# Kernel optimization log

Measured on AMD Instinct MI355X. Metric: run time of the kernel, lower is better.

## Reference

```python
import jax, jax.numpy as jnp
import numpy as np

B, NC, NF, D = 4, 256, 768, 768
TOK_RATIO = 0.5
LN_EPS = 1e-5


def _linear(x, w, b):
    # w: [D_in, D_out]
    return x @ w + b


def _leaky(x):
    return jax.nn.leaky_relu(x, negative_slope=0.01)


def setup_inputs() -> dict:
    key = jax.random.key(0)
    ks = jax.random.split(key, 12)
    s = 1.0 / np.sqrt(D)
    inp = {
        "cls_tokens": jax.random.normal(ks[0], (B, NC, D), dtype=jnp.float32),
        "feats": jax.random.normal(ks[1], (B, NF, D), dtype=jnp.float32),
        "W_head_w": jax.random.uniform(ks[2], (D, D), minval=-s, maxval=s),
        "W_head_b": jax.random.uniform(ks[3], (D,), minval=-s, maxval=s),
        "W_tail_w": jax.random.uniform(ks[4], (D, D), minval=-s, maxval=s),
        "W_tail_b": jax.random.uniform(ks[5], (D,), minval=-s, maxval=s),
        "lin1_w": jax.random.uniform(ks[6], (D, D), minval=-s, maxval=s),
        "lin1_b": jax.random.uniform(ks[7], (D,), minval=-s, maxval=s),
        "lin2_w": jax.random.uniform(ks[8], (D, D), minval=-s, maxval=s),
        "lin2_b": jax.random.uniform(ks[9], (D,), minval=-s, maxval=s),
        "ln_w": jnp.ones((D,), dtype=jnp.float32),
        "ln_b": jnp.zeros((D,), dtype=jnp.float32),
    }
    return inp


def reference(cls_tokens, feats, W_head_w, W_head_b, W_tail_w, W_tail_b,
              lin1_w, lin1_b, lin2_w, lin2_b, ln_w, ln_b):
    topk = int(TOK_RATIO * NC)
    scale = D ** (-0.5)

    # feats is detached in the original (clone().detach())
    x = jnp.concatenate([cls_tokens, jax.lax.stop_gradient(feats)], axis=1)  # [B, Nt, D]

    e_h = _linear(cls_tokens, W_head_w, W_head_b)  # [B, Nc, D]
    e_t = _linear(x, W_tail_w, W_tail_b)           # [B, Nt, D]

    attn_logit = jnp.einsum('bnd,bmd->bnm', e_h * scale, e_t)  # [B, Nc, Nt]
    topk_weight, topk_index = jax.lax.top_k(attn_logit, topk)  # [B, Nc, k]

    # Gather neighbor embeddings: Nb_h[b, n, j] = e_t[b, topk_index[b, n, j]]
    Nb_h = jax.vmap(lambda et, idx: et[idx])(e_t, topk_index)  # [B, Nc, k, D]

    topk_prob = jax.nn.softmax(topk_weight, axis=2)            # [B, Nc, k]
    p = topk_prob[..., None]
    eh_r = p * Nb_h + (1.0 - p) * e_h[:, :, None, :]           # [B, Nc, k, D]

    gate = jnp.tanh(e_h[:, :, None, :] + eh_r)
    ka_weight = jnp.einsum('bnkd,bnkd->bnk', Nb_h, gate)
    ka_prob = jax.nn.softmax(ka_weight, axis=2)
    e_Nh = jnp.einsum('bnk,bnkd->bnd', ka_prob, Nb_h)          # [B, Nc, D]

    # bi-interaction aggregation
    sum_emb = _leaky(_linear((e_h + e_Nh) * 0.1 + cls_tokens, lin1_w, lin1_b))
    bi_emb = _leaky(_linear(e_h * e_Nh * 0.1 + cls_tokens, lin2_w, lin2_b))
    embedding = sum_emb + bi_emb

    # LayerNorm (dropout is a no-op: p=0 and output overwritten in original)
    mu = jnp.mean(embedding, axis=-1, keepdims=True)
    var = jnp.var(embedding, axis=-1, keepdims=True)
    h = (embedding - mu) * jax.lax.rsqrt(var + LN_EPS) * ln_w + ln_b
    return h
```

## Files before the change

### kernel.cpp

```cpp
#include <hip/hip_runtime.h>
#include <hip/hip_bf16.h>
#include <math.h>

#define DDIM 768
#define NCLS 256
#define NFEAT 768
#define NTOK 1024
#define NBATCH 4
#define KSEL 128

typedef float f32x4 __attribute__((ext_vector_type(4)));
typedef short s16x8 __attribute__((ext_vector_type(8)));

__device__ __forceinline__ float wsum(float v) {
#pragma unroll
  for (int o = 32; o; o >>= 1) v += __shfl_down(v, o, 64);
  return v;
}
__device__ __forceinline__ float wmaxr(float v) {
#pragma unroll
  for (int o = 32; o; o >>= 1) v = fmaxf(v, __shfl_down(v, o, 64));
  return v;
}
__device__ __forceinline__ short f2bf(float f) {
  union { __hip_bfloat16 h; short s; } u;
  u.h = __float2bfloat16(f);
  return u.s;
}
__device__ __forceinline__ float bf2f(short s) {
  union { unsigned u; float f; } c;
  c.u = ((unsigned)(unsigned short)s) << 16;
  return c.f;
}
__device__ __forceinline__ void cvt8(float4 x, float4 y, s16x8& h, s16x8& l) {
  float v[8] = {x.x, x.y, x.z, x.w, y.x, y.y, y.z, y.w};
#pragma unroll
  for (int i = 0; i < 8; ++i) {
    short hh = f2bf(v[i]);
    h[i] = hh;
    l[i] = f2bf(v[i] - bf2f(hh));
  }
}
__device__ __forceinline__ int swz(int row, int chunk) {
  return (row << 5) + (((chunk ^ (row >> 1)) & 3) << 3);
}

__global__ __launch_bounds__(256) void prep_all(
    const float* __restrict__ cls, const float* __restrict__ feats,
    const float* __restrict__ w0, const float* __restrict__ w1,
    const float* __restrict__ w2, const float* __restrict__ w3,
    short* __restrict__ h0, short* __restrict__ h1, short* __restrict__ h2,
    short* __restrict__ h3, short* __restrict__ l0, short* __restrict__ l1,
    short* __restrict__ Xh, short* __restrict__ Xl) {
  __shared__ float tile[32][33];
  const int bid = blockIdx.x;
  const int t = threadIdx.x;
  if (bid < 2304) {
    const int z = bid / 576, rem = bid % 576;
    const int by = rem / 24, bx = rem % 24;
    const float* s = z == 0 ? w0 : z == 1 ? w1 : z == 2 ? w2 : w3;
    short* dh = z == 0 ? h0 : z == 1 ? h1 : z == 2 ? h2 : h3;
    short* dl = z == 0 ? l0 : z == 1 ? l1 : nullptr;
    const int tx = t & 31, ty0 = t >> 5;
    const int r0 = by * 32, c0 = bx * 32;
#pragma unroll
    for (int i = 0; i < 4; ++i) {
      int ty = ty0 + i * 8;
      tile[ty][tx] = s[(size_t)(r0 + ty) * DDIM + c0 + tx];
    }
    __syncthreads();
#pragma unroll
    for (int i = 0; i < 4; ++i) {
      int ty = ty0 + i * 8;
      float v = tile[tx][ty];
      short hh = f2bf(v);
      dh[(size_t)(c0 + ty) * DDIM + r0 + tx] = hh;
      if (dl) dl[(size_t)(c0 + ty) * DDIM + r0 + tx] = f2bf(v - bf2f(hh));
    }
  } else {
    const size_t base = ((size_t)(bid - 2304) * 256 + t) * 8;
    const int row = (int)(base / DDIM);
    const int col = (int)(base % DDIM);
    const int b = row >> 10, rr = row & 1023;
    const float* src =
        (rr < NCLS) ? cls + ((size_t)b * NCLS + rr) * DDIM + col
                    : feats + ((size_t)b * NFEAT + (rr - NCLS)) * DDIM + col;
    float4 a0 = *(const float4*)(src);
    float4 a1 = *(const float4*)(src + 4);
    s16x8 h, l;
    cvt8(a0, a1, h, l);
    *(s16x8*)(Xh + base) = h;
    *(s16x8*)(Xl + base) = l;
  }
}

__global__ __launch_bounds__(256) void gemm_front(
    const short* __restrict__ Xh, const short* __restrict__ Xl,
    const short* __restrict__ WhT_h, const short* __restrict__ WhT_l,
    const float* __restrict__ Whb, const short* __restrict__ WtT_h,
    const short* __restrict__ WtT_l, const float* __restrict__ Wtb,
    short* __restrict__ eh_hi, short* __restrict__ eh_lo,
    short* __restrict__ et_hi, short* __restrict__ et_lo) {
  __shared__ short Ah[128 * 32], Al[128 * 32];
  __shared__ short Bh[64 * 32], Bl[64 * 32];
  const int bid = blockIdx.x;
  const int xcd = bid & 7, idx = bid >> 3;
  const int ytile = xcd * 5 + idx / 12;
  const int xtile = idx % 12;
  const int t = threadIdx.x;
  const int row0 = ytile * 128, col0 = xtile * 64;
  const bool head = row0 < 1024;

  const int ar = t >> 1, ac = (t & 1) * 2;
  const int aw0 = swz(ar, ac), aw1 = swz(ar, ac + 1);
  size_t xrow;
  {
    int gr = row0 + ar;
    xrow = head ? (size_t)(((gr >> 8) << 10) + (gr & 255)) : (size_t)(gr - 1024);
  }
  const short* aph = Xh + xrow * DDIM + ac * 8;
  const short* apl = Xl + xrow * DDIM + ac * 8;
  const int br = t >> 2, bc = t & 3;
  const int bw0 = swz(br, bc);
  const short* bph = (head ? WhT_h : WtT_h) + (size_t)(col0 + br) * DDIM + bc * 8;
  const short* bpl = (head ? WhT_l : WtT_l) + (size_t)(col0 + br) * DDIM + bc * 8;
  const float* biasu = head ? Whb : Wtb;

  const int lane = t & 63, wave = t >> 6;
  const int wr = wave >> 1, wc = wave & 1;
  const int fr = lane & 15, fq = lane >> 4;

  f32x4 acc[4][2] = {};
  s16x8 rah0 = *(const s16x8*)(aph);
  s16x8 rah1 = *(const s16x8*)(aph + 8);
  s16x8 ral0 = *(const s16x8*)(apl);
  s16x8 ral1 = *(const s16x8*)(apl + 8);
  s16x8 rbh = *(const s16x8*)(bph);
  s16x8 rbl = *(const s16x8*)(bpl);

  for (int kt = 0; kt < 24; ++kt) {
    __syncthreads();
    *(s16x8*)&Ah[aw0] = rah0;
    *(s16x8*)&Ah[aw1] = rah1;
    *(s16x8*)&Al[aw0] = ral0;
    *(s16x8*)&Al[aw1] = ral1;
    *(s16x8*)&Bh[bw0] = rbh;
    *(s16x8*)&Bl[bw0] = rbl;
    __syncthreads();
    const int kn = (kt < 23 ? kt + 1 : 23) * 32;
    rah0 = *(const s16x8*)(aph + kn);
    rah1 = *(const s16x8*)(aph + kn + 8);
    ral0 = *(const s16x8*)(apl + kn);
    ral1 = *(const s16x8*)(apl + kn + 8);
    rbh = *(const s16x8*)(bph + kn);
    rbl = *(const s16x8*)(bpl + kn);

    s16x8 afh[4], afl[4];
#pragma unroll
    for (int m = 0; m < 4; ++m) {
      int ao = swz(wr * 64 + m * 16 + fr, fq);
      afh[m] = *(const s16x8*)&Ah[ao];
      afl[m] = *(const s16x8*)&Al[ao];
    }
#pragma unroll
    for (int n = 0; n < 2; ++n) {
      int bo = swz(wc * 32 + n * 16 + fr, fq);
      s16x8 bfh = *(const s16x8*)&Bh[bo];
      s16x8 bfl = *(const s16x8*)&Bl[bo];
#pragma unroll
      for (int m = 0; m < 4; ++m) {
        acc[m][n] =
            __builtin_amdgcn_mfma_f32_16x16x32_bf16(afh[m], bfh, acc[m][n], 0, 0, 0);
        acc[m][n] =
            __builtin_amdgcn_mfma_f32_16x16x32_bf16(afh[m], bfl, acc[m][n], 0, 0, 0);
        acc[m][n] =
            __builtin_amdgcn_mfma_f32_16x16x32_bf16(afl[m], bfh, acc[m][n], 0, 0, 0);
      }
    }
  }

  short* Ch = head ? eh_hi : et_hi;
  short* Cl = head ? eh_lo : et_lo;
  const int rbase = head ? row0 : row0 - 1024;
#pragma unroll
  for (int m = 0; m < 4; ++m) {
#pragma unroll
    for (int n = 0; n < 2; ++n) {
#pragma unroll
      for (int r = 0; r < 4; ++r) {
        int rg = rbase + wr * 64 + m * 16 + fq * 4 + r;
        int cg = col0 + wc * 32 + n * 16 + fr;
        float v = acc[m][n][r] + biasu[cg];
        size_t o = (size_t)rg * DDIM + cg;
        short hh = f2bf(v);
        Ch[o] = hh;
        Cl[o] = f2bf(v - bf2f(hh));
      }
    }
  }
}

__global__ __launch_bounds__(256) void gemm_logits(
    const short* __restrict__ eh_hi, const short* __restrict__ eh_lo,
    const short* __restrict__ et_hi, const short* __restrict__ et_lo,
    float* __restrict__ logits, float scale) {
  __shared__ short Ah[32 * 32], Al[32 * 32];
  __shared__ short Bh[64 * 32], Bl[64 * 32];
  const int bid = blockIdx.x;
  const int xcd = bid & 7, idx = bid >> 3;
  const int batch = xcd >> 1;
  const int sub = ((xcd & 1) << 6) | idx;
  const int xtile = sub & 15, ytile = sub >> 4;
  const int row0 = ytile * 32, col0 = xtile * 64;
  const int t = threadIdx.x;

  const int ahalf = t >> 7, ac2 = t & 127;
  const int asr = ac2 >> 2, acc_ = ac2 & 3;
  const short* aptr = (ahalf ? eh_lo : eh_hi) +
                      ((size_t)batch * NCLS + row0 + asr) * DDIM + acc_ * 8;
  const int aso = swz(asr, acc_);
  const int bsr = t >> 2, bcc = t & 3;
  const short* bph = et_hi + ((size_t)batch * NTOK + col0 + bsr) * DDIM + bcc * 8;
  const short* bpl = et_lo + ((size_t)batch * NTOK + col0 + bsr) * DDIM + bcc * 8;
  const int bso = swz(bsr, bcc);

  const int lane = t & 63, wave = t >> 6;
  const int wr = wave >> 1, wc = wave & 1;
  const int fr = lane & 15, fq = lane >> 4;

  f32x4 acc[2] = {};
  s16x8 rA = *(const s16x8*)(aptr);
  s16x8 rbh = *(const s16x8*)(bph);
  s16x8 rbl = *(const s16x8*)(bpl);

  for (int kt = 0; kt < 24; ++kt) {
    __syncthreads();
    *(s16x8*)&(ahalf ? Al : Ah)[aso] = rA;
    *(s16x8*)&Bh[bso] = rbh;
    *(s16x8*)&Bl[bso] = rbl;
    __syncthreads();
    const int kn = (kt < 23 ? kt + 1 : 23) * 32;
    rA = *(const s16x8*)(aptr + kn);
    rbh = *(const s16x8*)(bph + kn);
    rbl = *(const s16x8*)(bpl + kn);
    int ao = swz(wr * 16 + fr, fq);
    s16x8 afh = *(const s16x8*)&Ah[ao];
    s16x8 afl = *(const s16x8*)&Al[ao];
#pragma unroll
    for (int n = 0; n < 2; ++n) {
      int bo = swz(wc * 32 + n * 16 + fr, fq);
      s16x8 bfh = *(const s16x8*)&Bh[bo];
      s16x8 bfl = *(const s16x8*)&Bl[bo];
      acc[n] = __builtin_amdgcn_mfma_f32_16x16x32_bf16(afh, bfh, acc[n], 0, 0, 0);
      acc[n] = __builtin_amdgcn_mfma_f32_16x16x32_bf16(afh, bfl, acc[n], 0, 0, 0);
      acc[n] = __builtin_amdgcn_mfma_f32_16x16x32_bf16(afl, bfh, acc[n], 0, 0, 0);
    }
  }

  float* Cb = logits + (size_t)batch * NCLS * NTOK;
#pragma unroll
  for (int n = 0; n < 2; ++n)
#pragma unroll
    for (int r = 0; r < 4; ++r) {
      int rg = row0 + wr * 16 + fq * 4 + r;
      int cg = col0 + wc * 32 + n * 16 + fr;
      Cb[(size_t)rg * NTOK + cg] = scale * acc[n][r];
    }
}

__global__ __launch_bounds__(256) void gemm_lin(
    const short* __restrict__ inbf, const short* __restrict__ L1T,
    const short* __restrict__ L2T, const float* __restrict__ b1,
    const float* __restrict__ b2, float* __restrict__ emb) {
  __shared__ short A1[32 * 32], A2[32 * 32];
  __shared__ short B1[64 * 32], B2[64 * 32];
  const int bid = blockIdx.x;
  const int xcd = bid & 7, idx = bid >> 3;
  const int ytile = xcd * 4 + idx / 12, xtile = idx % 12;
  const int t = threadIdx.x;
  const int row0 = ytile * 32, col0 = xtile * 64;

  const int ahalf = t >> 7, at = t & 127;
  const int asr = at >> 2, asc = at & 3;
  const short* aptr = inbf + (ahalf ? (size_t)1024 * DDIM : 0) +
                      (size_t)(row0 + asr) * DDIM + asc * 8;
  const int aso = swz(asr, asc);
  const int bsr = t >> 2, bsc = t & 3;
  const short* b1p = L1T + (size_t)(col0 + bsr) * DDIM + bsc * 8;
  const short* b2p = L2T + (size_t)(col0 + bsr) * DDIM + bsc * 8;
  const int bso = swz(bsr, bsc);

  const int lane = t & 63, wave = t >> 6;
  const int wr = wave >> 1, wc = wave & 1;
  const int fr = lane & 15, fq = lane >> 4;

  f32x4 acc1[2] = {}, acc2[2] = {};
  s16x8 rA = *(const s16x8*)(aptr);
  s16x8 rB1 = *(const s16x8*)(b1p);
  s16x8 rB2 = *(const s16x8*)(b2p);
  for (int kt = 0; kt < 24; ++kt) {
    __syncthreads();
    *(s16x8*)&(ahalf ? A2 : A1)[aso] = rA;
    *(s16x8*)&B1[bso] = rB1;
    *(s16x8*)&B2[bso] = rB2;
    __syncthreads();
    const int kn = (kt < 23 ? kt + 1 : 23) * 32;
    rA = *(const s16x8*)(aptr + kn);
    rB1 = *(const s16x8*)(b1p + kn);
    rB2 = *(const s16x8*)(b2p + kn);
    int ao = swz(wr * 16 + fr, fq);
    s16x8 a1f = *(const s16x8*)&A1[ao];
    s16x8 a2f = *(const s16x8*)&A2[ao];
#pragma unroll
    for (int n = 0; n < 2; ++n) {
      int bo = swz(wc * 32 + n * 16 + fr, fq);
      s16x8 b1f = *(const s16x8*)&B1[bo];
      s16x8 b2f = *(const s16x8*)&B2[bo];
      acc1[n] = __builtin_amdgcn_mfma_f32_16x16x32_bf16(a1f, b1f, acc1[n], 0, 0, 0);
      acc2[n] = __builtin_amdgcn_mfma_f32_16x16x32_bf16(a2f, b2f, acc2[n], 0, 0, 0);
    }
  }
#pragma unroll
  for (int n = 0; n < 2; ++n)
#pragma unroll
    for (int r = 0; r < 4; ++r) {
      int rg = row0 + wr * 16 + fq * 4 + r;
      int cg = col0 + wc * 32 + n * 16 + fr;
      float v1 = acc1[n][r] + b1[cg];
      v1 = v1 > 0.f ? v1 : 0.01f * v1;
      float v2 = acc2[n][r] + b2[cg];
      v2 = v2 > 0.f ? v2 : 0.01f * v2;
      emb[(size_t)rg * DDIM + cg] = v1 + v2;
    }
}

__global__ __launch_bounds__(256) void topk_select(
    const float* __restrict__ logits, float* __restrict__ tw,
    int* __restrict__ ti) {
  const int row = blockIdx.x;
  const int t = threadIdx.x;
  const int lane = t & 63, wave = t >> 6;
  __shared__ int hist[256];
  __shared__ int sh_bin, sh_rem;
  __shared__ int cnt;
  __shared__ int wsumT[4];

  float4 v4 = *(const float4*)(logits + (size_t)row * NTOK + 4 * t);
  float val[4] = {v4.x, v4.y, v4.z, v4.w};
  unsigned key[4];
#pragma unroll
  for (int i = 0; i < 4; ++i) {
    unsigned u = __float_as_uint(val[i]);
    key[i] = (u & 0x80000000u) ? ~u : (u | 0x80000000u);
  }

  unsigned pref = 0, mask = 0;
  int rem = KSEL;
#pragma unroll
  for (int shift = 24; shift >= 0; shift -= 8) {
    hist[t] = 0;
    __syncthreads();
#pragma unroll
    for (int i = 0; i < 4; ++i)
      if ((key[i] & mask) == pref)
        atomicAdd(&hist[(key[i] >> shift) & 255], 1);
    __syncthreads();
    if (wave == 0) {
      int h0 = hist[4 * lane], h1 = hist[4 * lane + 1];
      int h2 = hist[4 * lane + 2], h3 = hist[4 * lane + 3];
      int s = h0 + h1 + h2 + h3;
#pragma unroll
      for (int o = 1; o < 64; o <<= 1) {
        int v = __shfl_down(s, o, 64);
        if (lane + o < 64) s += v;
      }
      int abv = __shfl_down(s, 1, 64);
      if (lane == 63) abv = 0;
      int c3 = abv + h3, c2 = c3 + h2, c1 = c2 + h1, c0 = c1 + h0;
      int bin = -1, nab = 0;
      if (c3 >= rem && abv < rem) { bin = 4 * lane + 3; nab = abv; }
      else if (c2 >= rem && c3 < rem) { bin = 4 * lane + 2; nab = c3; }
      else if (c1 >= rem && c2 < rem) { bin = 4 * lane + 1; nab = c2; }
      else if (c0 >= rem && c1 < rem) { bin = 4 * lane + 0; nab = c1; }
      if (bin >= 0) { sh_bin = bin; sh_rem = rem - nab; }
    }
    __syncthreads();
    pref |= ((unsigned)sh_bin) << shift;
    mask |= 0xFFu << shift;
    rem = sh_rem;
  }

  const unsigned T = pref;
  const int above = KSEL - rem;

  if (t == 0) cnt = 0;
  int tc = 0;
#pragma unroll
  for (int i = 0; i < 4; ++i) tc += (key[i] == T);
  int inc = tc;
#pragma unroll
  for (int o = 1; o < 64; o <<= 1) {
    int v = __shfl_up(inc, o, 64);
    if (lane >= o) inc += v;
  }
  if (lane == 63) wsumT[wave] = inc;
  __syncthreads();
  int wbase = 0;
#pragma unroll
  for (int w = 0; w < 4; ++w)
    if (w < wave) wbase += wsumT[w];
  int excl = wbase + inc - tc;

  float* twr = tw + (size_t)row * KSEL;
  int* tir = ti + (size_t)row * KSEL;
#pragma unroll
  for (int i = 0; i < 4; ++i) {
    if (key[i] > T) {
      int slot = atomicAdd(&cnt, 1);
      twr[slot] = val[i];
      tir[slot] = 4 * t + i;
    } else if (key[i] == T) {
      int r = excl++;
      if (r < rem) {
        twr[above + r] = val[i];
        tir[above + r] = 4 * t + i;
      }
    }
  }
}

__global__ __launch_bounds__(256) void agg1(const short* __restrict__ eh_hi,
                                            const short* __restrict__ et_hi,
                                            const float* __restrict__ tw,
                                            const int* __restrict__ ti,
                                            float* __restrict__ kaw_raw) {
  const int bid = blockIdx.x;
  const int xcd = bid & 7, slot = bid >> 3;
  const int batch = xcd >> 1;
  const int u = ((xcd & 1) << 8) | slot;
  const int row = batch * 256 + (u >> 1);
  const int half = u & 1;
  const int t = threadIdx.x, lane = t & 63, wave = t >> 6;
  __shared__ float p[KSEL];
  __shared__ int idxs[KSEL];
  __shared__ float red[2];

  if (t < KSEL) {
    p[t] = tw[(size_t)row * KSEL + t];
    idxs[t] = ti[(size_t)row * KSEL + t];
  }
  __syncthreads();
  if (wave == 0) {
    float m = wmaxr(fmaxf(p[lane], p[lane + 64]));
    if (!lane) red[0] = m;
  }
  __syncthreads();
  if (t < KSEL) p[t] = __expf(p[t] - red[0]);
  __syncthreads();
  if (wave == 0) {
    float s = wsum(p[lane] + p[lane + 64]);
    if (!lane) red[1] = s;
  }
  __syncthreads();
  if (t < KSEL) p[t] *= (1.f / red[1]);
  __syncthreads();

  float ehr[12];
  {
    const short* ehrow = eh_hi + (size_t)row * DDIM;
    s16x8 e8 = *(const s16x8*)(ehrow + 8 * lane);
    short4 e4 = *(const short4*)(ehrow + 512 + 4 * lane);
#pragma unroll
    for (int i = 0; i < 8; ++i) ehr[i] = bf2f(e8[i]);
    ehr[8] = bf2f(e4.x);
    ehr[9] = bf2f(e4.y);
    ehr[10] = bf2f(e4.z);
    ehr[11] = bf2f(e4.w);
  }
  const short* etb = et_hi + (size_t)batch * NTOK * DDIM;

  for (int i = 0; i < 16; ++i) {
    int j = half * 64 + wave * 16 + i;
    float pj = p[j];
    float a = 4.f - 2.f * pj, b2 = 2.f * pj;
    const short* nb = etb + (size_t)idxs[j] * DDIM;
    s16x8 n8 = *(const s16x8*)(nb + 8 * lane);
    short4 n4 = *(const short4*)(nb + 512 + 4 * lane);
    float nq[12];
#pragma unroll
    for (int q = 0; q < 8; ++q) nq[q] = bf2f(n8[q]);
    nq[8] = bf2f(n4.x);
    nq[9] = bf2f(n4.y);
    nq[10] = bf2f(n4.z);
    nq[11] = bf2f(n4.w);
    float partial = 0.f;
#pragma unroll
    for (int q = 0; q < 12; ++q) {
      float y2 = fmaf(a, ehr[q], b2 * nq[q]);
      float ex = __expf(y2);
      float g = fmaf(-2.f, __builtin_amdgcn_rcpf(1.f + ex), 1.f);
      partial = fmaf(nq[q], g, partial);
    }
    partial = wsum(partial);
    if (!lane) kaw_raw[(size_t)row * KSEL + j] = partial;
  }
}

__global__ __launch_bounds__(192) void agg2(
    const short* __restrict__ eh_hi, const short* __restrict__ et_hi,
    const float* __restrict__ cls, const float* __restrict__ kaw_raw,
    const int* __restrict__ ti, short* __restrict__ inbf) {
  const int bid = blockIdx.x;
  const int xcd = bid & 7, slot = bid >> 3;
  const int batch = xcd >> 1;
  const int row = batch * 256 + (xcd & 1) * 128 + slot;
  const int t = threadIdx.x, lane = t & 63, wave = t >> 6;
  __shared__ float kp[KSEL];
  __shared__ int idxs[KSEL];
  __shared__ float red[2];

  if (t < KSEL) {
    kp[t] = kaw_raw[(size_t)row * KSEL + t];
    idxs[t] = ti[(size_t)row * KSEL + t];
  }
  __syncthreads();
  if (wave == 0) {
    float m = wmaxr(fmaxf(kp[lane], kp[lane + 64]));
    if (!lane) red[0] = m;
  }
  __syncthreads();
  if (t < KSEL) kp[t] = __expf(kp[t] - red[0]);
  __syncthreads();
  if (wave == 0) {
    float s = wsum(kp[lane] + kp[lane + 64]);
    if (!lane) red[1] = s;
  }
  __syncthreads();
  if (t < KSEL) kp[t] *= (1.f / red[1]);
  __syncthreads();

  const size_t o = (size_t)row * DDIM + 4 * t;
  short4 ehs = *(const short4*)(eh_hi + o);
  float4 eh4 = {bf2f(ehs.x), bf2f(ehs.y), bf2f(ehs.z), bf2f(ehs.w)};
  float4 cl4 = *(const float4*)(cls + o);
  const short* etb = et_hi + (size_t)batch * NTOK * DDIM;

  float ax = 0.f, ay = 0.f, az = 0.f, aw = 0.f;
#pragma unroll 8
  for (int j = 0; j < KSEL; ++j) {
    float pr = kp[j];
    short4 nb = *(const short4*)(etb + (size_t)idxs[j] * DDIM + 4 * t);
    ax = fmaf(pr, bf2f(nb.x), ax);
    ay = fmaf(pr, bf2f(nb.y), ay);
    az = fmaf(pr, bf2f(nb.z), az);
    aw = fmaf(pr, bf2f(nb.w), aw);
  }

  short4 sv, bv;
  sv.x = f2bf((eh4.x + ax) * 0.1f + cl4.x);
  sv.y = f2bf((eh4.y + ay) * 0.1f + cl4.y);
  sv.z = f2bf((eh4.z + az) * 0.1f + cl4.z);
  sv.w = f2bf((eh4.w + aw) * 0.1f + cl4.w);
  bv.x = f2bf((eh4.x * ax) * 0.1f + cl4.x);
  bv.y = f2bf((eh4.y * ay) * 0.1f + cl4.y);
  bv.z = f2bf((eh4.z * az) * 0.1f + cl4.z);
  bv.w = f2bf((eh4.w * aw) * 0.1f + cl4.w);
  *(short4*)&inbf[o] = sv;
  *(short4*)&inbf[(size_t)(NBATCH * NCLS) * DDIM + o] = bv;
}

__global__ __launch_bounds__(256) void ln_kernel(const float* __restrict__ emb,
                                                 const float* __restrict__ lw,
                                                 const float* __restrict__ lb,
                                                 float* __restrict__ out) {
  const int row = blockIdx.x;
  const int t = threadIdx.x;
  const int lane = t & 63, wave = t >> 6;
  __shared__ float red[4];
  __shared__ float bs[2];
  float e[3];
#pragma unroll
  for (int c = 0; c < 3; ++c) e[c] = emb[(size_t)row * DDIM + t + 256 * c];
  float s = e[0] + e[1] + e[2];
  s = wsum(s);
  if (lane == 0) red[wave] = s;
  __syncthreads();
  if (t == 0) bs[0] = (red[0] + red[1] + red[2] + red[3]) * (1.f / DDIM);
  __syncthreads();
  float mu = bs[0];
  float q = 0.f;
#pragma unroll
  for (int c = 0; c < 3; ++c) {
    float d = e[c] - mu;
    q = fmaf(d, d, q);
  }
  q = wsum(q);
  if (lane == 0) red[wave] = q;
  __syncthreads();
  if (t == 0) bs[1] = (red[0] + red[1] + red[2] + red[3]) * (1.f / DDIM);
  __syncthreads();
  float rstd = rsqrtf(bs[1] + 1e-5f);
#pragma unroll
  for (int c = 0; c < 3; ++c) {
    int d = t + 256 * c;
    out[(size_t)row * DDIM + d] = (e[c] - mu) * rstd * lw[d] + lb[d];
  }
}

extern "C" void kernel_launch(void* const* d_in, const int* in_sizes, int n_in,
                              void* d_out, int out_size, void* d_ws,
                              size_t ws_size, hipStream_t stream) {
  const float* cls = (const float*)d_in[0];
  const float* feats = (const float*)d_in[1];
  const float* Whw = (const float*)d_in[2];
  const float* Whb = (const float*)d_in[3];
  const float* Wtw = (const float*)d_in[4];
  const float* Wtb = (const float*)d_in[5];
  const float* l1w = (const float*)d_in[6];
  const float* l1b = (const float*)d_in[7];
  const float* l2w = (const float*)d_in[8];
  const float* l2b = (const float*)d_in[9];
  const float* lnw = (const float*)d_in[10];
  const float* lnb = (const float*)d_in[11];
  float* out = (float*)d_out;

  float* ws = (float*)d_ws;
  float* emb = ws;
  short* eh_hi = (short*)(ws + 3932160);
  short* eh_lo = eh_hi + 786432;
  short* et_hi = (short*)(ws + 4718592);
  short* et_lo = et_hi + 3145728;
  short* WhT_h = (short*)(ws + 7864320);
  short* WhT_l = WhT_h + 589824;
  short* WtT_h = WhT_h + 2 * 589824;
  short* WtT_l = WhT_h + 3 * 589824;
  short* L1T = (short*)(ws + 9043968);
  short* L2T = L1T + 589824;
  float* logits = ws + 7864320;
  short* Xh = (short*)(ws + 9633792);
  short* Xl = Xh + 3145728;
  float* tw = ws + 9633792;
  int* ti = (int*)(ws + 9764864);
  float* kaw = ws + 9895936;
  short* inbf = (short*)(ws + 10027008);
  (void)ws_size;
  (void)in_sizes;
  (void)n_in;
  (void)out_size;

  const float scale = 0.036084391824351615f;
  dim3 blk(256);

  prep_all<<<dim3(3840), blk, 0, stream>>>(cls, feats, Whw, Wtw, l1w, l2w,
                                           WhT_h, WtT_h, L1T, L2T, WhT_l,
                                           WtT_l, Xh, Xl);
  gemm_front<<<dim3(480), blk, 0, stream>>>(
      Xh, Xl, WhT_h, WhT_l, Whb, WtT_h, WtT_l, Wtb, eh_hi, eh_lo, et_hi,
      et_lo);
  gemm_logits<<<dim3(512), blk, 0, stream>>>(eh_hi, eh_lo, et_hi, et_lo,
                                             logits, scale);
  topk_select<<<dim3(NBATCH * NCLS), blk, 0, stream>>>(logits, tw, ti);
  agg1<<<dim3(2048), blk, 0, stream>>>(eh_hi, et_hi, tw, ti, kaw);
  agg2<<<dim3(1024), dim3(192), 0, stream>>>(eh_hi, et_hi, cls, kaw, ti, inbf);
  gemm_lin<<<dim3(384), blk, 0, stream>>>(inbf, L1T, L2T, l1b, l2b, emb);
  ln_kernel<<<dim3(NBATCH * NCLS), blk, 0, stream>>>(emb, lnw, lnb, out);
}
```

Measured before the change: 124.2 us.

## Fuse top-k selection and both aggregation stages into one per-row kernel

Merges topk_select, agg1 and agg2 into a single select_agg kernel with one block per class row. Top-k weights and indices, gate scores and the second softmax now stay in shared memory instead of going through global buffers, and two launches disappear. In exchange, the agg1 work that used to be split across two blocks per row now runs in one block with twice the loop length, which halves parallelism in that phase. Only 192 of 256 threads take part in the final weighted-sum phase.

New measurement: 118.0 us. 5.0% less time.

```diff
diff --git a/kernel.cpp b/kernel.cpp
--- a/kernel.cpp
+++ b/kernel.cpp
@@ -268,82 +268,24 @@
     }
 }
 
-__global__ __launch_bounds__(256) void gemm_lin(
-    const short* __restrict__ inbf, const short* __restrict__ L1T,
-    const short* __restrict__ L2T, const float* __restrict__ b1,
-    const float* __restrict__ b2, float* __restrict__ emb) {
-  __shared__ short A1[32 * 32], A2[32 * 32];
-  __shared__ short B1[64 * 32], B2[64 * 32];
+__global__ __launch_bounds__(256) void select_agg(
+    const float* __restrict__ logits, const short* __restrict__ eh_hi,
+    const short* __restrict__ et_hi, const float* __restrict__ cls,
+    short* __restrict__ inbf) {
   const int bid = blockIdx.x;
-  const int xcd = bid & 7, idx = bid >> 3;
-  const int ytile = xcd * 4 + idx / 12, xtile = idx % 12;
-  const int t = threadIdx.x;
-  const int row0 = ytile * 32, col0 = xtile * 64;
-
-  const int ahalf = t >> 7, at = t & 127;
-  const int asr = at >> 2, asc = at & 3;
-  const short* aptr = inbf + (ahalf ? (size_t)1024 * DDIM : 0) +
-                      (size_t)(row0 + asr) * DDIM + asc * 8;
-  const int aso = swz(asr, asc);
-  const int bsr = t >> 2, bsc = t & 3;
-  const short* b1p = L1T + (size_t)(col0 + bsr) * DDIM + bsc * 8;
-  const short* b2p = L2T + (size_t)(col0 + bsr) * DDIM + bsc * 8;
-  const int bso = swz(bsr, bsc);
-
-  const int lane = t & 63, wave = t >> 6;
-  const int wr = wave >> 1, wc = wave & 1;
-  const int fr = lane & 15, fq = lane >> 4;
-
-  f32x4 acc1[2] = {}, acc2[2] = {};
-  s16x8 rA = *(const s16x8*)(aptr);
-  s16x8 rB1 = *(const s16x8*)(b1p);
-  s16x8 rB2 = *(const s16x8*)(b2p);
-  for (int kt = 0; kt < 24; ++kt) {
-    __syncthreads();
-    *(s16x8*)&(ahalf ? A2 : A1)[aso] = rA;
-    *(s16x8*)&B1[bso] = rB1;
-    *(s16x8*)&B2[bso] = rB2;
-    __syncthreads();
-    const int kn = (kt < 23 ? kt + 1 : 23) * 32;
-    rA = *(const s16x8*)(aptr + kn);
-    rB1 = *(const s16x8*)(b1p + kn);
-    rB2 = *(const s16x8*)(b2p + kn);
-    int ao = swz(wr * 16 + fr, fq);
-    s16x8 a1f = *(const s16x8*)&A1[ao];
-    s16x8 a2f = *(const s16x8*)&A2[ao];
-#pragma unroll
-    for (int n = 0; n < 2; ++n) {
-      int bo = swz(wc * 32 + n * 16 + fr, fq);
-      s16x8 b1f = *(const s16x8*)&B1[bo];
-      s16x8 b2f = *(const s16x8*)&B2[bo];
-      acc1[n] = __builtin_amdgcn_mfma_f32_16x16x32_bf16(a1f, b1f, acc1[n], 0, 0, 0);
-      acc2[n] = __builtin_amdgcn_mfma_f32_16x16x32_bf16(a2f, b2f, acc2[n], 0, 0, 0);
-    }
-  }
-#pragma unroll
-  for (int n = 0; n < 2; ++n)
-#pragma unroll
-    for (int r = 0; r < 4; ++r) {
-      int rg = row0 + wr * 16 + fq * 4 + r;
-      int cg = col0 + wc * 32 + n * 16 + fr;
-      float v1 = acc1[n][r] + b1[cg];
-      v1 = v1 > 0.f ? v1 : 0.01f * v1;
-      float v2 = acc2[n][r] + b2[cg];
-      v2 = v2 > 0.f ? v2 : 0.01f * v2;
-      emb[(size_t)rg * DDIM + cg] = v1 + v2;
-    }
-}
-
-__global__ __launch_bounds__(256) void topk_select(
-    const float* __restrict__ logits, float* __restrict__ tw,
-    int* __restrict__ ti) {
-  const int row = blockIdx.x;
-  const int t = threadIdx.x;
-  const int lane = t & 63, wave = t >> 6;
+  const int xcd = bid & 7, slot = bid >> 3;
+  const int batch = xcd >> 1;
+  const int row = batch * 256 + (xcd & 1) * 128 + slot;
+  const int t = threadIdx.x, lane = t & 63, wave = t >> 6;
+
   __shared__ int hist[256];
   __shared__ int sh_bin, sh_rem;
   __shared__ int cnt;
   __shared__ int wsumT[4];
+  __shared__ float p_sh[KSEL];
+  __shared__ int idx_sh[KSEL];
+  __shared__ float kaw_sh[KSEL];
+  __shared__ float red[2];
 
   float4 v4 = *(const float4*)(logits + (size_t)row * NTOK + 4 * t);
   float val[4] = {v4.x, v4.y, v4.z, v4.w};
@@ -353,7 +295,6 @@
     unsigned u = __float_as_uint(val[i]);
     key[i] = (u & 0x80000000u) ? ~u : (u | 0x80000000u);
   }
-
   unsigned pref = 0, mask = 0;
   int rem = KSEL;
 #pragma unroll
@@ -389,7 +330,6 @@
     mask |= 0xFFu << shift;
     rem = sh_rem;
   }
-
   const unsigned T = pref;
   const int above = KSEL - rem;
 
@@ -410,59 +350,35 @@
   for (int w = 0; w < 4; ++w)
     if (w < wave) wbase += wsumT[w];
   int excl = wbase + inc - tc;
-
-  float* twr = tw + (size_t)row * KSEL;
-  int* tir = ti + (size_t)row * KSEL;
 #pragma unroll
   for (int i = 0; i < 4; ++i) {
     if (key[i] > T) {
-      int slot = atomicAdd(&cnt, 1);
-      twr[slot] = val[i];
-      tir[slot] = 4 * t + i;
+      int s2 = atomicAdd(&cnt, 1);
+      p_sh[s2] = val[i];
+      idx_sh[s2] = 4 * t + i;
     } else if (key[i] == T) {
       int r = excl++;
       if (r < rem) {
-        twr[above + r] = val[i];
-        tir[above + r] = 4 * t + i;
+        p_sh[above + r] = val[i];
+        idx_sh[above + r] = 4 * t + i;
       }
     }
   }
-}
-
-__global__ __launch_bounds__(256) void agg1(const short* __restrict__ eh_hi,
-                                            const short* __restrict__ et_hi,
-                                            const float* __restrict__ tw,
-                                            const int* __restrict__ ti,
-                                            float* __restrict__ kaw_raw) {
-  const int bid = blockIdx.x;
-  const int xcd = bid & 7, slot = bid >> 3;
-  const int batch = xcd >> 1;
-  const int u = ((xcd & 1) << 8) | slot;
-  const int row = batch * 256 + (u >> 1);
-  const int half = u & 1;
-  const int t = threadIdx.x, lane = t & 63, wave = t >> 6;
-  __shared__ float p[KSEL];
-  __shared__ int idxs[KSEL];
-  __shared__ float red[2];
-
-  if (t < KSEL) {
-    p[t] = tw[(size_t)row * KSEL + t];
-    idxs[t] = ti[(size_t)row * KSEL + t];
-  }
-  __syncthreads();
+  __syncthreads();
+
   if (wave == 0) {
-    float m = wmaxr(fmaxf(p[lane], p[lane + 64]));
+    float m = wmaxr(fmaxf(p_sh[lane], p_sh[lane + 64]));
     if (!lane) red[0] = m;
   }
   __syncthreads();
-  if (t < KSEL) p[t] = __expf(p[t] - red[0]);
+  if (t < KSEL) p_sh[t] = __expf(p_sh[t] - red[0]);
   __syncthreads();
   if (wave == 0) {
-    float s = wsum(p[lane] + p[lane + 64]);
+    float s = wsum(p_sh[lane] + p_sh[lane + 64]);
     if (!lane) red[1] = s;
   }
   __syncthreads();
-  if (t < KSEL) p[t] *= (1.f / red[1]);
+  if (t < KSEL) p_sh[t] *= (1.f / red[1]);
   __syncthreads();
 
   float ehr[12];
@@ -479,11 +395,11 @@
   }
   const short* etb = et_hi + (size_t)batch * NTOK * DDIM;
 
-  for (int i = 0; i < 16; ++i) {
-    int j = half * 64 + wave * 16 + i;
-    float pj = p[j];
+  for (int i = 0; i < 32; ++i) {
+    int j = wave * 32 + i;
+    float pj = p_sh[j];
     float a = 4.f - 2.f * pj, b2 = 2.f * pj;
-    const short* nb = etb + (size_t)idxs[j] * DDIM;
+    const short* nb = etb + (size_t)idx_sh[j] * DDIM;
     s16x8 n8 = *(const s16x8*)(nb + 8 * lane);
     short4 n4 = *(const short4*)(nb + 512 + 4 * lane);
     float nq[12];
@@ -502,71 +418,118 @@
       partial = fmaf(nq[q], g, partial);
     }
     partial = wsum(partial);
-    if (!lane) kaw_raw[(size_t)row * KSEL + j] = partial;
-  }
-}
-
-__global__ __launch_bounds__(192) void agg2(
-    const short* __restrict__ eh_hi, const short* __restrict__ et_hi,
-    const float* __restrict__ cls, const float* __restrict__ kaw_raw,
-    const int* __restrict__ ti, short* __restrict__ inbf) {
+    if (!lane) kaw_sh[j] = partial;
+  }
+  __syncthreads();
+
+  if (wave == 0) {
+    float m = wmaxr(fmaxf(kaw_sh[lane], kaw_sh[lane + 64]));
+    if (!lane) red[0] = m;
+  }
+  __syncthreads();
+  if (t < KSEL) kaw_sh[t] = __expf(kaw_sh[t] - red[0]);
+  __syncthreads();
+  if (wave == 0) {
+    float s = wsum(kaw_sh[lane] + kaw_sh[lane + 64]);
+    if (!lane) red[1] = s;
+  }
+  __syncthreads();
+  if (t < KSEL) kaw_sh[t] *= (1.f / red[1]);
+  __syncthreads();
+
+  if (t < 192) {
+    const size_t o = (size_t)row * DDIM + 4 * t;
+    short4 ehs = *(const short4*)(eh_hi + o);
+    float4 eh4 = {bf2f(ehs.x), bf2f(ehs.y), bf2f(ehs.z), bf2f(ehs.w)};
+    float4 cl4 = *(const float4*)(cls + o);
+    float ax = 0.f, ay = 0.f, az = 0.f, aw = 0.f;
+#pragma unroll 8
+    for (int j = 0; j < KSEL; ++j) {
+      float pr = kaw_sh[j];
+      short4 nb = *(const short4*)(etb + (size_t)idx_sh[j] * DDIM + 4 * t);
+      ax = fmaf(pr, bf2f(nb.x), ax);
+      ay = fmaf(pr, bf2f(nb.y), ay);
+      az = fmaf(pr, bf2f(nb.z), az);
+      aw = fmaf(pr, bf2f(nb.w), aw);
+    }
+    short4 sv, bv;
+    sv.x = f2bf((eh4.x + ax) * 0.1f + cl4.x);
+    sv.y = f2bf((eh4.y + ay) * 0.1f + cl4.y);
+    sv.z = f2bf((eh4.z + az) * 0.1f + cl4.z);
+    sv.w = f2bf((eh4.w + aw) * 0.1f + cl4.w);
+    bv.x = f2bf((eh4.x * ax) * 0.1f + cl4.x);
+    bv.y = f2bf((eh4.y * ay) * 0.1f + cl4.y);
+    bv.z = f2bf((eh4.z * az) * 0.1f + cl4.z);
+    bv.w = f2bf((eh4.w * aw) * 0.1f + cl4.w);
+    *(short4*)&inbf[o] = sv;
+    *(short4*)&inbf[(size_t)(NBATCH * NCLS) * DDIM + o] = bv;
+  }
+}
+
+__global__ __launch_bounds__(256) void gemm_lin(
+    const short* __restrict__ inbf, const short* __restrict__ L1T,
+    const short* __restrict__ L2T, const float* __restrict__ b1,
+    const float* __restrict__ b2, float* __restrict__ emb) {
+  __shared__ short A1[32 * 32], A2[32 * 32];
+  __shared__ short B1[64 * 32], B2[64 * 32];
   const int bid = blockIdx.x;
-  const int xcd = bid & 7, slot = bid >> 3;
-  const int batch = xcd >> 1;
-  const int row = batch * 256 + (xcd & 1) * 128 + slot;
-  const int t = threadIdx.x, lane = t & 63, wave = t >> 6;
-  __shared__ float kp[KSEL];
-  __shared__ int idxs[KSEL];
-  __shared__ float red[2];
-
-  if (t < KSEL) {
-    kp[t] = kaw_raw[(size_t)row * KSEL + t];
-    idxs[t] = ti[(size_t)row * KSEL + t];
-  }
-  __syncthreads();
-  if (wave == 0) {
-    float m = wmaxr(fmaxf(kp[lane], kp[lane + 64]));
-    if (!lane) red[0] = m;
-  }
-  __syncthreads();
-  if (t < KSEL) kp[t] = __expf(kp[t] - red[0]);
-  __syncthreads();
-  if (wave == 0) {
-    float s = wsum(kp[lane] + kp[lane + 64]);
-    if (!lane) red[1] = s;
-  }
-  __syncthreads();
-  if (t < KSEL) kp[t] *= (1.f / red[1]);
-  __syncthreads();
-
-  const size_t o = (size_t)row * DDIM + 4 * t;
-  short4 ehs = *(const short4*)(eh_hi + o);
-  float4 eh4 = {bf2f(ehs.x), bf2f(ehs.y), bf2f(ehs.z), bf2f(ehs.w)};
-  float4 cl4 = *(const float4*)(cls + o);
-  const short* etb = et_hi + (size_t)batch * NTOK * DDIM;
-
-  float ax = 0.f, ay = 0.f, az = 0.f, aw = 0.f;
-#pragma unroll 8
-  for (int j = 0; j < KSEL; ++j) {
-    float pr = kp[j];
-    short4 nb = *(const short4*)(etb + (size_t)idxs[j] * DDIM + 4 * t);
-    ax = fmaf(pr, bf2f(nb.x), ax);
-    ay = fmaf(pr, bf2f(nb.y), ay);
-    az = fmaf(pr, bf2f(nb.z), az);
-    aw = fmaf(pr, bf2f(nb.w), aw);
-  }
-
-  short4 sv, bv;
-  sv.x = f2bf((eh4.x + ax) * 0.1f + cl4.x);
-  sv.y = f2bf((eh4.y + ay) * 0.1f + cl4.y);
-  sv.z = f2bf((eh4.z + az) * 0.1f + cl4.z);
-  sv.w = f2bf((eh4.w + aw) * 0.1f + cl4.w);
-  bv.x = f2bf((eh4.x * ax) * 0.1f + cl4.x);
-  bv.y = f2bf((eh4.y * ay) * 0.1f + cl4.y);
-  bv.z = f2bf((eh4.z * az) * 0.1f + cl4.z);
-  bv.w = f2bf((eh4.w * aw) * 0.1f + cl4.w);
-  *(short4*)&inbf[o] = sv;
-  *(short4*)&inbf[(size_t)(NBATCH * NCLS) * DDIM + o] = bv;
+  const int xcd = bid & 7, idx = bid >> 3;
+  const int ytile = xcd * 4 + idx / 12, xtile = idx % 12;
+  const int t = threadIdx.x;
+  const int row0 = ytile * 32, col0 = xtile * 64;
+
+  const int ahalf = t >> 7, at = t & 127;
+  const int asr = at >> 2, asc = at & 3;
+  const short* aptr = inbf + (ahalf ? (size_t)1024 * DDIM : 0) +
+                      (size_t)(row0 + asr) * DDIM + asc * 8;
+  const int aso = swz(asr, asc);
+  const int bsr = t >> 2, bsc = t & 3;
+  const short* b1p = L1T + (size_t)(col0 + bsr) * DDIM + bsc * 8;
+  const short* b2p = L2T + (size_t)(col0 + bsr) * DDIM + bsc * 8;
+  const int bso = swz(bsr, bsc);
+
+  const int lane = t & 63, wave = t >> 6;
+  const int wr = wave >> 1, wc = wave & 1;
+  const int fr = lane & 15, fq = lane >> 4;
+
+  f32x4 acc1[2] = {}, acc2[2] = {};
+  s16x8 rA = *(const s16x8*)(aptr);
+  s16x8 rB1 = *(const s16x8*)(b1p);
+  s16x8 rB2 = *(const s16x8*)(b2p);
+  for (int kt = 0; kt < 24; ++kt) {
+    __syncthreads();
+    *(s16x8*)&(ahalf ? A2 : A1)[aso] = rA;
+    *(s16x8*)&B1[bso] = rB1;
+    *(s16x8*)&B2[bso] = rB2;
+    __syncthreads();
+    const int kn = (kt < 23 ? kt + 1 : 23) * 32;
+    rA = *(const s16x8*)(aptr + kn);
+    rB1 = *(const s16x8*)(b1p + kn);
+    rB2 = *(const s16x8*)(b2p + kn);
+    int ao = swz(wr * 16 + fr, fq);
+    s16x8 a1f = *(const s16x8*)&A1[ao];
+    s16x8 a2f = *(const s16x8*)&A2[ao];
+#pragma unroll
+    for (int n = 0; n < 2; ++n) {
+      int bo = swz(wc * 32 + n * 16 + fr, fq);
+      s16x8 b1f = *(const s16x8*)&B1[bo];
+      s16x8 b2f = *(const s16x8*)&B2[bo];
+      acc1[n] = __builtin_amdgcn_mfma_f32_16x16x32_bf16(a1f, b1f, acc1[n], 0, 0, 0);
+      acc2[n] = __builtin_amdgcn_mfma_f32_16x16x32_bf16(a2f, b2f, acc2[n], 0, 0, 0);
+    }
+  }
+#pragma unroll
+  for (int n = 0; n < 2; ++n)
+#pragma unroll
+    for (int r = 0; r < 4; ++r) {
+      int rg = row0 + wr * 16 + fq * 4 + r;
+      int cg = col0 + wc * 32 + n * 16 + fr;
+      float v1 = acc1[n][r] + b1[cg];
+      v1 = v1 > 0.f ? v1 : 0.01f * v1;
+      float v2 = acc2[n][r] + b2[cg];
+      v2 = v2 > 0.f ? v2 : 0.01f * v2;
+      emb[(size_t)rg * DDIM + cg] = v1 + v2;
+    }
 }
 
 __global__ __launch_bounds__(256) void ln_kernel(const float* __restrict__ emb,
@@ -639,9 +602,6 @@
   float* logits = ws + 7864320;
   short* Xh = (short*)(ws + 9633792);
   short* Xl = Xh + 3145728;
-  float* tw = ws + 9633792;
-  int* ti = (int*)(ws + 9764864);
-  float* kaw = ws + 9895936;
   short* inbf = (short*)(ws + 10027008);
   (void)ws_size;
   (void)in_sizes;
@@ -659,9 +619,7 @@
       et_lo);
   gemm_logits<<<dim3(512), blk, 0, stream>>>(eh_hi, eh_lo, et_hi, et_lo,
                                              logits, scale);
-  topk_select<<<dim3(NBATCH * NCLS), blk, 0, stream>>>(logits, tw, ti);
-  agg1<<<dim3(2048), blk, 0, stream>>>(eh_hi, et_hi, tw, ti, kaw);
-  agg2<<<dim3(1024), dim3(192), 0, stream>>>(eh_hi, et_hi, cls, kaw, ti, inbf);
+  select_agg<<<dim3(1024), blk, 0, stream>>>(logits, eh_hi, et_hi, cls, inbf);
   gemm_lin<<<dim3(384), blk, 0, stream>>>(inbf, L1T, L2T, l1b, l2b, emb);
   ln_kernel<<<dim3(NBATCH * NCLS), blk, 0, stream>>>(emb, lnw, lnb, out);
 }
```
